# Performance work log

Hardware: AMD Instinct MI355X
Metric: run time of the kernel (lower is better)

## Reference

```python
import jax, jax.numpy as jnp
import numpy as np

NUM_BUCKETS = 64
MAX_DISTANCE = 50000.0


def setup_inputs() -> dict:
    R, I, N, E, H = 64, 512, 4, 256, 8
    key = jax.random.key(0)
    ks = jax.random.split(key, 12)
    p = lambda k, shape: (jax.random.normal(k, shape, dtype=jnp.float32) * 0.02)
    return {
        "x": jax.random.normal(ks[0], (R, I, N, E), dtype=jnp.float32),
        "distances": jax.random.randint(ks[1], (N, I, I), 0, 50000).astype(jnp.int32),
        "Wq": p(ks[2], (E, E)), "bq": jnp.zeros((E,), jnp.float32),
        "Wk": p(ks[3], (E, E)), "bk": jnp.zeros((E,), jnp.float32),
        "Wv": p(ks[4], (E, E)), "bv": jnp.zeros((E,), jnp.float32),
        "Wo": p(ks[5], (E, E)), "bo": jnp.zeros((E,), jnp.float32),
        "rel_emb": p(ks[6], (NUM_BUCKETS, H)),
    }


def reference(x, distances, Wq, bq, Wk, bk, Wv, bv, Wo, bo, rel_emb):
    R, I, N, E = x.shape
    H = rel_emb.shape[1]
    D = E // H
    # scaling = head_dim**-0.5 / sqrt(num_rows)
    scaling = (D ** -0.5) / np.sqrt(R)

    def proj(W, b):
        return (jnp.einsum('rine,fe->rinf', x, W) + b).reshape(R, I, N, H, D)

    q = proj(Wq, bq) * scaling
    k = proj(Wk, bk)
    v = proj(Wv, bv)

    # Row-summed attention logits: (H, N, I, J)
    attn_weights = jnp.einsum('rinhd,rjnhd->hnij', q, k)

    # T5-style relative position bias (buckets = linspace boundaries)
    buckets = jnp.linspace(0.0, MAX_DISTANCE, NUM_BUCKETS - 1)
    abs_dist = jnp.abs(distances).astype(jnp.float32)
    # torch.bucketize(right=False) == searchsorted side='left'
    bucket_idx = jnp.searchsorted(buckets, abs_dist, side='left')  # (N, I, J)
    bias = rel_emb[bucket_idx]                  # (N, I, J, H)
    attn_weights = attn_weights + jnp.transpose(bias, (3, 0, 1, 2))

    attn_probs = jax.nn.softmax(attn_weights, axis=-1)  # dropout p=0.0 -> identity

    context = jnp.einsum('hnij,rjnhd->rinhd', attn_probs, v).reshape(R, I, N, E)
    output = jnp.einsum('rine,fe->rinf', context, Wo) + bo
    return output, attn_probs
```

## Files before the change

### kernel.cpp

```cpp
#include <hip/hip_runtime.h>

typedef unsigned short u16;
typedef unsigned int u32;
typedef float f32x4 __attribute__((ext_vector_type(4)));
typedef short bf16x8 __attribute__((ext_vector_type(8)));
typedef unsigned short u16x8 __attribute__((ext_vector_type(8)));

#define SL 33554432u

__device__ __forceinline__ float bf2f(u16 u) {
  u32 v = ((u32)u) << 16;
  return __builtin_bit_cast(float, v);
}
__device__ __forceinline__ u16 f2bf(float f) {
  u32 i = __builtin_bit_cast(u32, f);
  i += 0x7fffu + ((i >> 16) & 1u);
  return (u16)(i >> 16);
}

#define GLDS16(g, l) __builtin_amdgcn_global_load_lds( \
    (const __attribute__((address_space(1))) void*)(g), \
    (__attribute__((address_space(3))) void*)(l), 16, 0, 0)

__device__ __forceinline__ void stage128(const u16* gbase, int ldk, u16* lds, int tid) {
  #pragma unroll
  for (int rep = 0; rep < 4; ++rep) {
    int c = tid + rep * 256;
    int row = c >> 3, slot = c & 7;
    const u16* g = gbase + (size_t)row * ldk + ((slot ^ (row & 7)) << 3);
    GLDS16(g, lds + c * 8);
  }
}

template <bool SWAP>
__device__ __forceinline__ void mfma128(const u16* As, const u16* Bs, int lane,
                                        int wm0, int wn0, f32x4 acc[4][4]) {
  #pragma unroll
  for (int kk = 0; kk < 2; ++kk) {
    bf16x8 a[4], b[4];
    #pragma unroll
    for (int mi = 0; mi < 4; ++mi) {
      int r = wm0 + mi * 16 + (lane & 15);
      int c16 = (kk * 4 + (lane >> 4)) ^ (r & 7);
      a[mi] = *(const bf16x8*)(As + r * 64 + c16 * 8);
    }
    #pragma unroll
    for (int ni = 0; ni < 4; ++ni) {
      int r = wn0 + ni * 16 + (lane & 15);
      int c16 = (kk * 4 + (lane >> 4)) ^ (r & 7);
      b[ni] = *(const bf16x8*)(Bs + r * 64 + c16 * 8);
    }
    #pragma unroll
    for (int mi = 0; mi < 4; ++mi)
      #pragma unroll
      for (int ni = 0; ni < 4; ++ni)
        acc[mi][ni] = SWAP
          ? __builtin_amdgcn_mfma_f32_16x16x32_bf16(b[ni], a[mi], acc[mi][ni], 0, 0, 0)
          : __builtin_amdgcn_mfma_f32_16x16x32_bf16(a[mi], b[ni], acc[mi][ni], 0, 0, 0);
  }
}

template <bool SWAP>
__device__ __forceinline__ void gemm_core(const u16* A, int ldkA, const u16* B, int ldkB,
                                          int NT, u16* As, u16* Bs,
                                          int tid, int lane, int wm0, int wn0,
                                          f32x4 acc[4][4]) {
  for (int t = 0; t < NT; ++t) {
    stage128(A + t * 64, ldkA, As, tid);
    stage128(B + t * 64, ldkB, Bs, tid);
    __syncthreads();
    mfma128<SWAP>(As, Bs, lane, wm0, wn0, acc);
    __syncthreads();
  }
}

__global__ __launch_bounds__(256) void k_castx(const float* __restrict__ src,
                                               u16* __restrict__ dst) {
  int idx = blockIdx.x * 256 + threadIdx.x;
  const float4* s = (const float4*)src;
  float4 a = s[(size_t)idx * 2], b = s[(size_t)idx * 2 + 1];
  u16x8 o;
  o[0] = f2bf(a.x); o[1] = f2bf(a.y); o[2] = f2bf(a.z); o[3] = f2bf(a.w);
  o[4] = f2bf(b.x); o[5] = f2bf(b.y); o[6] = f2bf(b.z); o[7] = f2bf(b.w);
  *(u16x8*)(dst + (size_t)idx * 8) = o;
}

__global__ __launch_bounds__(256) void k_castw(
    const float* __restrict__ Wq, const float* __restrict__ Wk,
    const float* __restrict__ Wv, const float* __restrict__ Wo,
    u16* __restrict__ Wb) {
  int idx = blockIdx.x * 256 + threadIdx.x;
  int w = idx >> 13, off = idx & 8191;
  const float* src = (w == 0) ? Wq : (w == 1) ? Wk : (w == 2) ? Wv : Wo;
  const float4* s = (const float4*)(src + (size_t)off * 8);
  float4 a = s[0], b = s[1];
  u16x8 o;
  o[0] = f2bf(a.x); o[1] = f2bf(a.y); o[2] = f2bf(a.z); o[3] = f2bf(a.w);
  o[4] = f2bf(b.x); o[5] = f2bf(b.y); o[6] = f2bf(b.z); o[7] = f2bf(b.w);
  *(u16x8*)(Wb + (size_t)w * 65536 + (size_t)off * 8) = o;
}

__global__ __launch_bounds__(256) void k_proj_mm(
    const u16* __restrict__ xb, const u16* __restrict__ Wb,
    const float* __restrict__ bq, const float* __restrict__ bk, const float* __restrict__ bv,
    u16* __restrict__ qt, u16* __restrict__ kt, u16* __restrict__ vt, float scaling) {
  __shared__ __align__(16) u16 As[128 * 64];
  __shared__ __align__(16) u16 Bs[128 * 64];
  const int tid = threadIdx.x, lane = tid & 63, wave = tid >> 6;
  const int wm0 = (wave >> 1) * 64, wn0 = (wave & 1) * 64;
  const int m0 = blockIdx.x * 128, n0 = blockIdx.y * 128, w = blockIdx.z;

  f32x4 acc[4][4];
  #pragma unroll
  for (int mi = 0; mi < 4; ++mi)
    #pragma unroll
    for (int ni = 0; ni < 4; ++ni) acc[mi][ni] = (f32x4){0.f, 0.f, 0.f, 0.f};

  gemm_core<true>(xb + (size_t)m0 * 256, 256, Wb + w * 65536 + (size_t)n0 * 256, 256,
                  4, As, Bs, tid, lane, wm0, wn0, acc);

  const float* bias = (w == 0) ? bq : (w == 1) ? bk : bv;
  u16* dst = (w == 0) ? qt : (w == 1) ? kt : vt;
  const float sc = (w == 0) ? scaling : 1.0f;

  #pragma unroll
  for (int ni = 0; ni < 4; ++ni) {
    int f = n0 + wn0 + ni * 16 + (lane >> 4) * 4;
    int h = f >> 5, d = f & 31;
    float4 bb = *(const float4*)(bias + f);
    #pragma unroll
    for (int mi = 0; mi < 4; ++mi) {
      int m = m0 + wm0 + mi * 16 + (lane & 15);
      int n = m & 3, i = (m >> 2) & 511, r = m >> 11;
      size_t o = ((size_t)((n * 8 + h) * 512 + i)) * 2048 + r * 32 + d;
      ushort4 wv4;
      wv4.x = f2bf((acc[mi][ni][0] + bb.x) * sc);
      wv4.y = f2bf((acc[mi][ni][1] + bb.y) * sc);
      wv4.z = f2bf((acc[mi][ni][2] + bb.z) * sc);
      wv4.w = f2bf((acc[mi][ni][3] + bb.w) * sc);
      *(ushort4*)(dst + o) = wv4;
    }
  }
}

__global__ __launch_bounds__(256) void k_attn_mm(
    const u16* __restrict__ qt, const u16* __restrict__ kt, u16* __restrict__ lgt) {
  __shared__ __align__(16) u16 As[128 * 64];
  __shared__ __align__(16) u16 Bs[128 * 64];
  const int tid = threadIdx.x, lane = tid & 63, wave = tid >> 6;
  const int wm0 = (wave >> 1) * 64, wn0 = (wave & 1) * 64;
  const int bid = blockIdx.x;
  const int sb = (bid & 7) * 64 + (bid >> 3);
  const int nh = sb >> 4, tt = sb & 15;
  const int m0 = (tt >> 2) * 128, n0 = (tt & 3) * 128;

  f32x4 acc[4][4];
  #pragma unroll
  for (int mi = 0; mi < 4; ++mi)
    #pragma unroll
    for (int ni = 0; ni < 4; ++ni) acc[mi][ni] = (f32x4){0.f, 0.f, 0.f, 0.f};

  const size_t base = (size_t)nh * 512 * 2048;
  gemm_core<true>(qt + base + (size_t)m0 * 2048, 2048, kt + base + (size_t)n0 * 2048, 2048,
                  32, As, Bs, tid, lane, wm0, wn0, acc);

  #pragma unroll
  for (int mi = 0; mi < 4; ++mi) {
    int row = m0 + wm0 + mi * 16 + (lane & 15);
    #pragma unroll
    for (int ni = 0; ni < 4; ++ni) {
      int col = n0 + wn0 + ni * 16 + (lane >> 4) * 4;
      ushort4 wv4;
      wv4.x = f2bf(acc[mi][ni][0]);
      wv4.y = f2bf(acc[mi][ni][1]);
      wv4.z = f2bf(acc[mi][ni][2]);
      wv4.w = f2bf(acc[mi][ni][3]);
      *(ushort4*)(lgt + (size_t)nh * 262144 + (size_t)row * 512 + col) = wv4;
    }
  }
}

__global__ __launch_bounds__(256) void k_softmax(
    const u16* __restrict__ lgt, const int* __restrict__ dist, const float* __restrict__ rel,
    float* __restrict__ probs, u16* __restrict__ pbf) {
  const int t = threadIdx.x;
  const int lane = t & 63, wv = t >> 6;
  const int b = blockIdx.x;
  const int i = b & 511, n = b >> 9;

  const int* dr = dist + ((size_t)n * 512 + i) * 512 + lane * 8;
  int4 dA = *(const int4*)dr, dB = *(const int4*)(dr + 4);
  int dd[8] = {dA.x, dA.y, dA.z, dA.w, dB.x, dB.y, dB.z, dB.w};
  int u[8];
  #pragma unroll
  for (int j = 0; j < 8; ++j) {
    int v = dd[j] < 0 ? -dd[j] : dd[j];
    int q = (62 * v + 49999) / 50000; if (q > 63) q = 63;
    u[j] = q;
  }

  #pragma unroll
  for (int hh = 0; hh < 2; ++hh) {
    const int h = wv * 2 + hh;
    const int nh = n * 8 + h;
    const u16* lr = lgt + ((size_t)nh * 512 + i) * 512 + lane * 8;
    u16x8 L = *(const u16x8*)lr;
    float vj[8];
    float mx = -1e30f;
    #pragma unroll
    for (int j = 0; j < 8; ++j) {
      vj[j] = bf2f(L[j]) + rel[u[j] * 8 + h];
      mx = fmaxf(mx, vj[j]);
    }
    #pragma unroll
    for (int off = 32; off; off >>= 1) mx = fmaxf(mx, __shfl_xor(mx, off));
    float s = 0.f;
    #pragma unroll
    for (int j = 0; j < 8; ++j) { vj[j] = __expf(vj[j] - mx); s += vj[j]; }
    #pragma unroll
    for (int off = 32; off; off >>= 1) s += __shfl_xor(s, off);
    float inv = 1.0f / s;
    float4 pa, pb;
    pa.x = vj[0]*inv; pa.y = vj[1]*inv; pa.z = vj[2]*inv; pa.w = vj[3]*inv;
    pb.x = vj[4]*inv; pb.y = vj[5]*inv; pb.z = vj[6]*inv; pb.w = vj[7]*inv;
    size_t po = ((size_t)(h * 4 + n) * 512 + i) * 512 + lane * 8;
    *(float4*)(probs + po) = pa;
    *(float4*)(probs + po + 4) = pb;
    u16x8 pc;
    pc[0]=f2bf(pa.x); pc[1]=f2bf(pa.y); pc[2]=f2bf(pa.z); pc[3]=f2bf(pa.w);
    pc[4]=f2bf(pb.x); pc[5]=f2bf(pb.y); pc[6]=f2bf(pb.z); pc[7]=f2bf(pb.w);
    size_t pq = ((size_t)nh * 512 + i) * 512 + lane * 8;
    *(u16x8*)(pbf + pq) = pc;
  }
}

__global__ __launch_bounds__(256) void k_vtrans(const u16* __restrict__ vt, u16* __restrict__ vtt) {
  __shared__ u16 ts[64][72];
  const int b = blockIdx.x;
  const int ct_ = b & 31, it = (b >> 5) & 7, nh = b >> 8;
  const int i0 = it * 64, c0 = ct_ * 64;
  const int t = threadIdx.x;
  #pragma unroll
  for (int rep = 0; rep < 2; ++rep) {
    int c = t + rep * 256;
    int r = c >> 3, q = c & 7;
    u16x8 v = *(const u16x8*)(vt + ((size_t)nh * 512 + i0 + r) * 2048 + c0 + q * 8);
    #pragma unroll
    for (int j = 0; j < 8; ++j) ts[r][q * 8 + j] = v[j];
  }
  __syncthreads();
  #pragma unroll
  for (int rep = 0; rep < 2; ++rep) {
    int c = t + rep * 256;
    int rr = c >> 3, q = c & 7;
    u16x8 o;
    #pragma unroll
    for (int j = 0; j < 8; ++j) o[j] = ts[q * 8 + j][rr];
    *(u16x8*)(vtt + ((size_t)nh * 2048 + c0 + rr) * 512 + i0 + q * 8) = o;
  }
}

__global__ __launch_bounds__(256) void k_ctx_mm(
    const u16* __restrict__ vtt, const u16* __restrict__ pbf, u16* __restrict__ ct) {
  __shared__ __align__(16) u16 As[128 * 64];
  __shared__ __align__(16) u16 Bs[128 * 64];
  const int tid = threadIdx.x, lane = tid & 63, wave = tid >> 6;
  const int wm0 = (wave >> 1) * 64, wn0 = (wave & 1) * 64;
  const int bid = blockIdx.x;
  const int sb = (bid & 7) * 256 + (bid >> 3);
  const int nh = sb >> 6, tt = sb & 63;
  const int m0 = (tt >> 2) * 128, n0 = (tt & 3) * 128;
  const int n = nh >> 3, h = nh & 7;

  f32x4 acc[4][4];
  #pragma unroll
  for (int mi = 0; mi < 4; ++mi)
    #pragma unroll
    for (int ni = 0; ni < 4; ++ni) acc[mi][ni] = (f32x4){0.f, 0.f, 0.f, 0.f};

  gemm_core<false>(vtt + (size_t)nh * 1048576 + (size_t)m0 * 512, 512,
                   pbf + (size_t)nh * 262144 + (size_t)n0 * 512, 512,
                   8, As, Bs, tid, lane, wm0, wn0, acc);

  #pragma unroll
  for (int mi = 0; mi < 4; ++mi) {
    int c_g = m0 + wm0 + mi * 16 + (lane >> 4) * 4;
    int rr = c_g >> 5, d = c_g & 31;
    #pragma unroll
    for (int ni = 0; ni < 4; ++ni) {
      int i_g = n0 + wn0 + ni * 16 + (lane & 15);
      size_t o = ((size_t)((rr * 512 + i_g) * 4 + n)) * 256 + h * 32 + d;
      ushort4 wv4;
      wv4.x = f2bf(acc[mi][ni][0]);
      wv4.y = f2bf(acc[mi][ni][1]);
      wv4.z = f2bf(acc[mi][ni][2]);
      wv4.w = f2bf(acc[mi][ni][3]);
      *(ushort4*)(ct + o) = wv4;
    }
  }
}

__global__ __launch_bounds__(256) void k_oproj_mm(
    const u16* __restrict__ ct, const u16* __restrict__ Wob,
    const float* __restrict__ bo, float* __restrict__ out) {
  __shared__ __align__(16) u16 As[128 * 64];
  __shared__ __align__(16) u16 Bs[128 * 64];
  const int tid = threadIdx.x, lane = tid & 63, wave = tid >> 6;
  const int wm0 = (wave >> 1) * 64, wn0 = (wave & 1) * 64;
  const int bid = blockIdx.x;
  const int sb = (bid & 7) * 256 + (bid >> 3);
  const int m0 = (sb >> 1) * 128, n0 = (sb & 1) * 128;

  f32x4 acc[4][4];
  #pragma unroll
  for (int mi = 0; mi < 4; ++mi)
    #pragma unroll
    for (int ni = 0; ni < 4; ++ni) acc[mi][ni] = (f32x4){0.f, 0.f, 0.f, 0.f};

  gemm_core<true>(ct + (size_t)m0 * 256, 256, Wob + (size_t)n0 * 256, 256,
                  4, As, Bs, tid, lane, wm0, wn0, acc);

  #pragma unroll
  for (int ni = 0; ni < 4; ++ni) {
    int col = n0 + wn0 + ni * 16 + (lane >> 4) * 4;
    float4 bb = *(const float4*)(bo + col);
    #pragma unroll
    for (int mi = 0; mi < 4; ++mi) {
      int row = m0 + wm0 + mi * 16 + (lane & 15);
      float4 wv4;
      wv4.x = acc[mi][ni][0] + bb.x;
      wv4.y = acc[mi][ni][1] + bb.y;
      wv4.z = acc[mi][ni][2] + bb.z;
      wv4.w = acc[mi][ni][3] + bb.w;
      *(float4*)(out + (size_t)row * 256 + col) = wv4;
    }
  }
}

extern "C" void kernel_launch(void* const* d_in, const int* in_sizes, int n_in,
                              void* d_out, int out_size, void* d_ws, size_t ws_size,
                              hipStream_t stream) {
  const float* x  = (const float*)d_in[0];
  const int* dist = (const int*)d_in[1];
  const float* Wq = (const float*)d_in[2];
  const float* bq = (const float*)d_in[3];
  const float* Wk = (const float*)d_in[4];
  const float* bk = (const float*)d_in[5];
  const float* Wv = (const float*)d_in[6];
  const float* bv = (const float*)d_in[7];
  const float* Wo = (const float*)d_in[8];
  const float* bo = (const float*)d_in[9];
  const float* rel = (const float*)d_in[10];
  float* out = (float*)d_out;
  float* probs = out + (size_t)SL;

  u16* ws = (u16*)d_ws;
  u16* xb  = ws;
  u16* qt  = ws + (size_t)SL;
  u16* kt  = ws + (size_t)2 * SL;
  u16* vt  = ws + (size_t)3 * SL;
  u16* lgt = xb;
  u16* pbf = qt;
  u16* vtt = kt;
  u16* ctb = xb;
  u16* Wb  = ws + (size_t)4 * SL;

  const float scaling = 0.022097086912079608f;

  k_castx  <<<16384, 256, 0, stream>>>(x, xb);
  k_castw  <<<128, 256, 0, stream>>>(Wq, Wk, Wv, Wo, Wb);
  k_proj_mm<<<dim3(1024, 2, 3), 256, 0, stream>>>(xb, Wb, bq, bk, bv, qt, kt, vt, scaling);
  k_attn_mm<<<512, 256, 0, stream>>>(qt, kt, lgt);
  k_softmax<<<2048, 256, 0, stream>>>(lgt, dist, rel, probs, pbf);
  k_vtrans <<<8192, 256, 0, stream>>>(vt, vtt);
  k_ctx_mm <<<2048, 256, 0, stream>>>(vtt, pbf, ctb);
  k_oproj_mm<<<2048, 256, 0, stream>>>(ctb, Wb + 196608, bo, out);
}
```

Baseline: 367.4 us.

## Fuse x bf16 cast into projection GEMM and stage ctx epilogue through LDS

Removes the separate x-to-bf16 cast kernel by having the projection GEMM load fp32 x directly, convert it, and keep the whole 128x256 A tile in LDS. Each block reuses that tile across the Q, K and V weights, which drops the extra 64MB bf16 round trip and the triple re-read of x. The context GEMM epilogue now transposes through LDS so it can emit 16-byte contiguous stores instead of scattered 8-byte ones. The cost is larger LDS per block in the projection (80KB), which lowers occupancy, and serial work over the three weights inside each block.

```diff
diff --git a/kernel.cpp b/kernel.cpp
--- a/kernel.cpp
+++ b/kernel.cpp
@@ -72,17 +72,6 @@
     mfma128<SWAP>(As, Bs, lane, wm0, wn0, acc);
     __syncthreads();
   }
-}
-
-__global__ __launch_bounds__(256) void k_castx(const float* __restrict__ src,
-                                               u16* __restrict__ dst) {
-  int idx = blockIdx.x * 256 + threadIdx.x;
-  const float4* s = (const float4*)src;
-  float4 a = s[(size_t)idx * 2], b = s[(size_t)idx * 2 + 1];
-  u16x8 o;
-  o[0] = f2bf(a.x); o[1] = f2bf(a.y); o[2] = f2bf(a.z); o[3] = f2bf(a.w);
-  o[4] = f2bf(b.x); o[5] = f2bf(b.y); o[6] = f2bf(b.z); o[7] = f2bf(b.w);
-  *(u16x8*)(dst + (size_t)idx * 8) = o;
 }
 
 __global__ __launch_bounds__(256) void k_castw(
@@ -101,44 +90,71 @@
 }
 
 __global__ __launch_bounds__(256) void k_proj_mm(
-    const u16* __restrict__ xb, const u16* __restrict__ Wb,
+    const float* __restrict__ x, const u16* __restrict__ Wb,
     const float* __restrict__ bq, const float* __restrict__ bk, const float* __restrict__ bv,
     u16* __restrict__ qt, u16* __restrict__ kt, u16* __restrict__ vt, float scaling) {
-  __shared__ __align__(16) u16 As[128 * 64];
-  __shared__ __align__(16) u16 Bs[128 * 64];
+  __shared__ __align__(16) u16 As[4 * 8192];
+  __shared__ __align__(16) u16 Bs[8192];
   const int tid = threadIdx.x, lane = tid & 63, wave = tid >> 6;
   const int wm0 = (wave >> 1) * 64, wn0 = (wave & 1) * 64;
-  const int m0 = blockIdx.x * 128, n0 = blockIdx.y * 128, w = blockIdx.z;
-
-  f32x4 acc[4][4];
-  #pragma unroll
-  for (int mi = 0; mi < 4; ++mi)
-    #pragma unroll
-    for (int ni = 0; ni < 4; ++ni) acc[mi][ni] = (f32x4){0.f, 0.f, 0.f, 0.f};
-
-  gemm_core<true>(xb + (size_t)m0 * 256, 256, Wb + w * 65536 + (size_t)n0 * 256, 256,
-                  4, As, Bs, tid, lane, wm0, wn0, acc);
-
-  const float* bias = (w == 0) ? bq : (w == 1) ? bk : bv;
-  u16* dst = (w == 0) ? qt : (w == 1) ? kt : vt;
-  const float sc = (w == 0) ? scaling : 1.0f;
-
-  #pragma unroll
-  for (int ni = 0; ni < 4; ++ni) {
-    int f = n0 + wn0 + ni * 16 + (lane >> 4) * 4;
-    int h = f >> 5, d = f & 31;
-    float4 bb = *(const float4*)(bias + f);
-    #pragma unroll
-    for (int mi = 0; mi < 4; ++mi) {
-      int m = m0 + wm0 + mi * 16 + (lane & 15);
-      int n = m & 3, i = (m >> 2) & 511, r = m >> 11;
-      size_t o = ((size_t)((n * 8 + h) * 512 + i)) * 2048 + r * 32 + d;
-      ushort4 wv4;
-      wv4.x = f2bf((acc[mi][ni][0] + bb.x) * sc);
-      wv4.y = f2bf((acc[mi][ni][1] + bb.y) * sc);
-      wv4.z = f2bf((acc[mi][ni][2] + bb.z) * sc);
-      wv4.w = f2bf((acc[mi][ni][3] + bb.w) * sc);
-      *(ushort4*)(dst + o) = wv4;
+  const int bid = blockIdx.x;
+  const int sb = (bid & 7) * 256 + (bid >> 3);
+  const int mt = sb >> 1, n0 = (sb & 1) * 128;
+  const int m0 = mt * 128;
+
+  {
+    const float* xp = x + (size_t)m0 * 256;
+    #pragma unroll
+    for (int it = 0; it < 16; ++it) {
+      int g = tid + it * 256;
+      int row = g >> 5, col8 = g & 31;
+      int ktp = col8 >> 3, slot = col8 & 7;
+      const float* src = xp + row * 256 + col8 * 8;
+      float4 a = *(const float4*)src, b = *(const float4*)(src + 4);
+      u16x8 o;
+      o[0]=f2bf(a.x); o[1]=f2bf(a.y); o[2]=f2bf(a.z); o[3]=f2bf(a.w);
+      o[4]=f2bf(b.x); o[5]=f2bf(b.y); o[6]=f2bf(b.z); o[7]=f2bf(b.w);
+      *(u16x8*)(As + ktp * 8192 + row * 64 + ((slot ^ (row & 7)) << 3)) = o;
+    }
+  }
+
+  #pragma unroll 1
+  for (int w = 0; w < 3; ++w) {
+    f32x4 acc[4][4];
+    #pragma unroll
+    for (int mi = 0; mi < 4; ++mi)
+      #pragma unroll
+      for (int ni = 0; ni < 4; ++ni) acc[mi][ni] = (f32x4){0.f, 0.f, 0.f, 0.f};
+
+    const u16* Bw = Wb + w * 65536 + (size_t)n0 * 256;
+    for (int ktt = 0; ktt < 4; ++ktt) {
+      stage128(Bw + ktt * 64, 256, Bs, tid);
+      __syncthreads();
+      mfma128<true>(As + ktt * 8192, Bs, lane, wm0, wn0, acc);
+      __syncthreads();
+    }
+
+    const float* bias = (w == 0) ? bq : (w == 1) ? bk : bv;
+    u16* dst = (w == 0) ? qt : (w == 1) ? kt : vt;
+    const float sc = (w == 0) ? scaling : 1.0f;
+
+    #pragma unroll
+    for (int ni = 0; ni < 4; ++ni) {
+      int f = n0 + wn0 + ni * 16 + (lane >> 4) * 4;
+      int h = f >> 5, d = f & 31;
+      float4 bb = *(const float4*)(bias + f);
+      #pragma unroll
+      for (int mi = 0; mi < 4; ++mi) {
+        int m = m0 + wm0 + mi * 16 + (lane & 15);
+        int n = m & 3, i = (m >> 2) & 511, r = m >> 11;
+        size_t o = ((size_t)((n * 8 + h) * 512 + i)) * 2048 + r * 32 + d;
+        ushort4 wv4;
+        wv4.x = f2bf((acc[mi][ni][0] + bb.x) * sc);
+        wv4.y = f2bf((acc[mi][ni][1] + bb.y) * sc);
+        wv4.z = f2bf((acc[mi][ni][2] + bb.z) * sc);
+        wv4.w = f2bf((acc[mi][ni][3] + bb.w) * sc);
+        *(ushort4*)(dst + o) = wv4;
+      }
     }
   }
 }
@@ -262,8 +278,10 @@
 
 __global__ __launch_bounds__(256) void k_ctx_mm(
     const u16* __restrict__ vtt, const u16* __restrict__ pbf, u16* __restrict__ ct) {
-  __shared__ __align__(16) u16 As[128 * 64];
-  __shared__ __align__(16) u16 Bs[128 * 64];
+  __shared__ __align__(16) u16 lds[16640];
+  u16* As = lds;
+  u16* Bs = lds + 8192;
+  u16* ts = lds;
   const int tid = threadIdx.x, lane = tid & 63, wave = tid >> 6;
   const int wm0 = (wave >> 1) * 64, wn0 = (wave & 1) * 64;
   const int bid = blockIdx.x;
@@ -283,20 +301,27 @@
                    8, As, Bs, tid, lane, wm0, wn0, acc);
 
   #pragma unroll
-  for (int mi = 0; mi < 4; ++mi) {
-    int c_g = m0 + wm0 + mi * 16 + (lane >> 4) * 4;
-    int rr = c_g >> 5, d = c_g & 31;
+  for (int mi = 0; mi < 4; ++mi)
     #pragma unroll
     for (int ni = 0; ni < 4; ++ni) {
-      int i_g = n0 + wn0 + ni * 16 + (lane & 15);
-      size_t o = ((size_t)((rr * 512 + i_g) * 4 + n)) * 256 + h * 32 + d;
-      ushort4 wv4;
-      wv4.x = f2bf(acc[mi][ni][0]);
-      wv4.y = f2bf(acc[mi][ni][1]);
-      wv4.z = f2bf(acc[mi][ni][2]);
-      wv4.w = f2bf(acc[mi][ni][3]);
-      *(ushort4*)(ct + o) = wv4;
-    }
+      int i_l = wn0 + ni * 16 + (lane & 15);
+      #pragma unroll
+      for (int q = 0; q < 4; ++q) {
+        int c_l = wm0 + mi * 16 + (lane >> 4) * 4 + q;
+        ts[i_l * 130 + c_l] = f2bf(acc[mi][ni][q]);
+      }
+    }
+  __syncthreads();
+  #pragma unroll
+  for (int cc = 0; cc < 2; ++cc) {
+    int ch = tid + cc * 256;
+    int i_l = ch & 127, r_l = ch >> 7;
+    const u16* src = ts + i_l * 130 + r_l * 32;
+    int rr = (m0 >> 5) + r_l;
+    size_t o = ((size_t)((rr * 512 + n0 + i_l) * 4 + n)) * 256 + h * 32;
+    #pragma unroll
+    for (int j = 0; j < 4; ++j)
+      *(u16x8*)(ct + o + j * 8) = *(const u16x8*)(src + j * 8);
   }
 }
 
@@ -355,21 +380,19 @@
   float* probs = out + (size_t)SL;
 
   u16* ws = (u16*)d_ws;
-  u16* xb  = ws;
+  u16* lgt = ws;
   u16* qt  = ws + (size_t)SL;
   u16* kt  = ws + (size_t)2 * SL;
   u16* vt  = ws + (size_t)3 * SL;
-  u16* lgt = xb;
   u16* pbf = qt;
   u16* vtt = kt;
-  u16* ctb = xb;
+  u16* ctb = lgt;
   u16* Wb  = ws + (size_t)4 * SL;
 
   const float scaling = 0.022097086912079608f;
 
-  k_castx  <<<16384, 256, 0, stream>>>(x, xb);
   k_castw  <<<128, 256, 0, stream>>>(Wq, Wk, Wv, Wo, Wb);
-  k_proj_mm<<<dim3(1024, 2, 3), 256, 0, stream>>>(xb, Wb, bq, bk, bv, qt, kt, vt, scaling);
+  k_proj_mm<<<2048, 256, 0, stream>>>(x, Wb, bq, bk, bv, qt, kt, vt, scaling);
   k_attn_mm<<<512, 256, 0, stream>>>(qt, kt, lgt);
   k_softmax<<<2048, 256, 0, stream>>>(lgt, dist, rel, probs, pbf);
   k_vtrans <<<8192, 256, 0, stream>>>(vt, vtt);
```

After: 381.9 us. 1.04x slower.

## Coalesce projection and context epilogue stores via transposed fragments and LDS staging

Applied to the files above, without the earlier changes.

The QKV projection kernel now uses the other gemm_core accumulator orientation, so the 16 lanes of a group write consecutive d elements as scalar bf16 stores instead of scattered ushort4 stores. The context GEMM stages its bf16 output tile in a padded LDS buffer that reuses the A/B tile space. It then writes 64-byte contiguous rows with 16-byte vector stores instead of strided 8-byte stores. The intent is to cut uncoalesced global write traffic in both epilogues, at the cost of an extra barrier and LDS round-trip. The 260-byte padded row stride means the 16-byte LDS vector reads are not 16-byte aligned.

```diff
diff --git a/kernel.cpp b/kernel.cpp
--- a/kernel.cpp
+++ b/kernel.cpp
@@ -116,31 +116,28 @@
     #pragma unroll
     for (int ni = 0; ni < 4; ++ni) acc[mi][ni] = (f32x4){0.f, 0.f, 0.f, 0.f};
 
-  gemm_core<true>(xb + (size_t)m0 * 256, 256, Wb + w * 65536 + (size_t)n0 * 256, 256,
-                  4, As, Bs, tid, lane, wm0, wn0, acc);
+  gemm_core<false>(xb + (size_t)m0 * 256, 256, Wb + w * 65536 + (size_t)n0 * 256, 256,
+                   4, As, Bs, tid, lane, wm0, wn0, acc);
 
   const float* bias = (w == 0) ? bq : (w == 1) ? bk : bv;
   u16* dst = (w == 0) ? qt : (w == 1) ? kt : vt;
   const float sc = (w == 0) ? scaling : 1.0f;
 
   #pragma unroll
-  for (int ni = 0; ni < 4; ++ni) {
-    int f = n0 + wn0 + ni * 16 + (lane >> 4) * 4;
-    int h = f >> 5, d = f & 31;
-    float4 bb = *(const float4*)(bias + f);
-    #pragma unroll
-    for (int mi = 0; mi < 4; ++mi) {
-      int m = m0 + wm0 + mi * 16 + (lane & 15);
-      int n = m & 3, i = (m >> 2) & 511, r = m >> 11;
-      size_t o = ((size_t)((n * 8 + h) * 512 + i)) * 2048 + r * 32 + d;
-      ushort4 wv4;
-      wv4.x = f2bf((acc[mi][ni][0] + bb.x) * sc);
-      wv4.y = f2bf((acc[mi][ni][1] + bb.y) * sc);
-      wv4.z = f2bf((acc[mi][ni][2] + bb.z) * sc);
-      wv4.w = f2bf((acc[mi][ni][3] + bb.w) * sc);
-      *(ushort4*)(dst + o) = wv4;
-    }
-  }
+  for (int mi = 0; mi < 4; ++mi)
+    #pragma unroll
+    for (int ni = 0; ni < 4; ++ni) {
+      int f = n0 + wn0 + ni * 16 + (lane & 15);
+      int h = f >> 5, d = f & 31;
+      float bb = bias[f];
+      #pragma unroll
+      for (int q = 0; q < 4; ++q) {
+        int m = m0 + wm0 + mi * 16 + (lane >> 4) * 4 + q;
+        int n = m & 3, i = (m >> 2) & 511, r = m >> 11;
+        size_t o = ((size_t)((n * 8 + h) * 512 + i)) * 2048 + r * 32 + d;
+        dst[o] = f2bf((acc[mi][ni][q] + bb) * sc);
+      }
+    }
 }
 
 __global__ __launch_bounds__(256) void k_attn_mm(
@@ -262,8 +259,10 @@
 
 __global__ __launch_bounds__(256) void k_ctx_mm(
     const u16* __restrict__ vtt, const u16* __restrict__ pbf, u16* __restrict__ ct) {
-  __shared__ __align__(16) u16 As[128 * 64];
-  __shared__ __align__(16) u16 Bs[128 * 64];
+  __shared__ __align__(16) u16 lds[16640];
+  u16* As = lds;
+  u16* Bs = lds + 8192;
+  u16* ts = lds;
   const int tid = threadIdx.x, lane = tid & 63, wave = tid >> 6;
   const int wm0 = (wave >> 1) * 64, wn0 = (wave & 1) * 64;
   const int bid = blockIdx.x;
@@ -283,20 +282,27 @@
                    8, As, Bs, tid, lane, wm0, wn0, acc);
 
   #pragma unroll
-  for (int mi = 0; mi < 4; ++mi) {
-    int c_g = m0 + wm0 + mi * 16 + (lane >> 4) * 4;
-    int rr = c_g >> 5, d = c_g & 31;
+  for (int mi = 0; mi < 4; ++mi)
     #pragma unroll
     for (int ni = 0; ni < 4; ++ni) {
-      int i_g = n0 + wn0 + ni * 16 + (lane & 15);
-      size_t o = ((size_t)((rr * 512 + i_g) * 4 + n)) * 256 + h * 32 + d;
-      ushort4 wv4;
-      wv4.x = f2bf(acc[mi][ni][0]);
-      wv4.y = f2bf(acc[mi][ni][1]);
-      wv4.z = f2bf(acc[mi][ni][2]);
-      wv4.w = f2bf(acc[mi][ni][3]);
-      *(ushort4*)(ct + o) = wv4;
-    }
+      int i_l = wn0 + ni * 16 + (lane & 15);
+      #pragma unroll
+      for (int q = 0; q < 4; ++q) {
+        int c_l = wm0 + mi * 16 + (lane >> 4) * 4 + q;
+        ts[i_l * 130 + c_l] = f2bf(acc[mi][ni][q]);
+      }
+    }
+  __syncthreads();
+  #pragma unroll
+  for (int cc = 0; cc < 2; ++cc) {
+    int ch = tid + cc * 256;
+    int i_l = ch & 127, r_l = ch >> 7;
+    const u16* src = ts + i_l * 130 + r_l * 32;
+    int rr = (m0 >> 5) + r_l;
+    size_t o = ((size_t)((rr * 512 + n0 + i_l) * 4 + n)) * 256 + h * 32;
+    #pragma unroll
+    for (int j = 0; j < 4; ++j)
+      *(u16x8*)(ct + o + j * 8) = *(const u16x8*)(src + j * 8);
   }
 }
 
```

Result: no change. 362.9 us (-1.2%).
